# Optimization experiments

Hardware: AMD Instinct MI355X
Metric: run time of the kernel (lower is better)

## Reference

```python
import jax, jax.numpy as jnp
import numpy as np

SAMPLES = 300000
B = 256
D = 128
NEG = 1024
TEMP = 0.07
MOMENTUM = 0.5
EPS = 1e-12


def _l2n(x):
    # torch F.normalize(p=2, dim=1) semantics
    n = jnp.sqrt(jnp.sum(x * x, axis=-1, keepdims=True))
    return x / jnp.maximum(n, EPS)


def setup_inputs() -> dict:
    key = jax.random.key(0)
    k1, k2, k3, k4, k5, k6 = jax.random.split(key, 6)
    return {
        "audio_emb": jax.random.normal(k1, (B, D), dtype=jnp.float32),
        "video_emb": jax.random.normal(k2, (B, D), dtype=jnp.float32),
        "audio_memory": _l2n(jax.random.normal(k3, (SAMPLES, D), dtype=jnp.float32)),
        "video_memory": _l2n(jax.random.normal(k4, (SAMPLES, D), dtype=jnp.float32)),
        "indices": jax.random.randint(k5, (B,), 0, SAMPLES, dtype=jnp.int64),
        "neg_samples": jax.random.randint(k6, (B, NEG), 0, SAMPLES - 1, dtype=jnp.int64),
    }


def _scores(ctx, pos, neg):
    # ctx [B,D], pos [B,D], neg [B,NEG,D] -> [B, 1+NEG]
    s_pos = jnp.sum(pos * ctx, axis=-1, keepdims=True) / TEMP           # [B,1]
    s_neg = jnp.einsum("bnd,bd->bn", neg, ctx) / TEMP                   # [B,NEG]
    return jnp.concatenate([s_pos, s_neg], axis=1)


def reference(audio_emb, video_emb, audio_memory, video_memory, indices, neg_samples):
    na = _l2n(audio_emb)  # [B,D]
    nv = _l2n(video_emb)

    # alias sampling over uniform probs == uniform randint; shift to skip positive
    neg_idx = neg_samples + (neg_samples >= indices[:, None]).astype(neg_samples.dtype)

    pos_a = audio_memory[indices]      # [B,D]
    pos_v = video_memory[indices]
    neg_a = audio_memory[neg_idx]      # [B,NEG,D]
    neg_v = video_memory[neg_idx]

    # score order: (inter)audio_video, (inter)video_audio, (intra)audio, (intra)video
    scores = jnp.stack([
        _scores(na, pos_v, neg_v),
        _scores(nv, pos_a, neg_a),
        _scores(na, pos_a, neg_a),
        _scores(nv, pos_v, neg_v),
    ], axis=0)  # [4, B, 1+NEG]

    # momentum memory update (no-grad in original): gather -> mix -> normalize -> scatter
    new_a = _l2n(pos_a * MOMENTUM + na * (1.0 - MOMENTUM))
    new_v = _l2n(pos_v * MOMENTUM + nv * (1.0 - MOMENTUM))
    audio_memory_new = audio_memory.at[indices].set(new_a)
    video_memory_new = video_memory.at[indices].set(new_v)

    return scores, audio_memory_new, video_memory_new
```

## Files before the change

kernel.cpp:

```cpp
#include <hip/hip_runtime.h>

#define B 256
#define D 128
#define NEG 1024
#define SAMPLES 300000
#define TEMP 0.07f
#define EPS 1e-12f

constexpr int SCORES_ELEMS = 4 * B * (NEG + 1);
constexpr int MEM_ELEMS    = SAMPLES * D;

__device__ inline float wave_reduce_sum(float x) {
    #pragma unroll
    for (int off = 32; off > 0; off >>= 1) x += __shfl_xor(x, off, 64);
    return x;
}

__global__ __launch_bounds__(64) void prep_kernel(
    const float* __restrict__ audio_emb, const float* __restrict__ video_emb,
    const float* __restrict__ a_mem, const float* __restrict__ v_mem,
    const int* __restrict__ indices,
    float* __restrict__ na, float* __restrict__ nv,
    float* __restrict__ new_a, float* __restrict__ new_v,
    float* __restrict__ scores)
{
    const int b = blockIdx.x;
    const int l = threadIdx.x;

    float2 a = ((const float2*)(audio_emb + b * D))[l];
    float2 v = ((const float2*)(video_emb + b * D))[l];

    float sa = wave_reduce_sum(a.x * a.x + a.y * a.y);
    float sv = wave_reduce_sum(v.x * v.x + v.y * v.y);
    float ira = 1.0f / fmaxf(sqrtf(sa), EPS);
    float irv = 1.0f / fmaxf(sqrtf(sv), EPS);
    float2 naf = {a.x * ira, a.y * ira};
    float2 nvf = {v.x * irv, v.y * irv};
    ((float2*)(na + b * D))[l] = naf;
    ((float2*)(nv + b * D))[l] = nvf;

    const long long idx = (long long)indices[b];
    float2 pa = ((const float2*)(a_mem + idx * D))[l];
    float2 pv = ((const float2*)(v_mem + idx * D))[l];

    float d0 = wave_reduce_sum(pv.x * naf.x + pv.y * naf.y);
    float d1 = wave_reduce_sum(pa.x * nvf.x + pa.y * nvf.y);
    float d2 = wave_reduce_sum(pa.x * naf.x + pa.y * naf.y);
    float d3 = wave_reduce_sum(pv.x * nvf.x + pv.y * nvf.y);
    if (l == 0) {
        scores[(0 * B + b) * (NEG + 1)] = d0 / TEMP;
        scores[(1 * B + b) * (NEG + 1)] = d1 / TEMP;
        scores[(2 * B + b) * (NEG + 1)] = d2 / TEMP;
        scores[(3 * B + b) * (NEG + 1)] = d3 / TEMP;
    }

    float2 ta = {0.5f * (pa.x + naf.x), 0.5f * (pa.y + naf.y)};
    float2 tv = {0.5f * (pv.x + nvf.x), 0.5f * (pv.y + nvf.y)};
    float sta = wave_reduce_sum(ta.x * ta.x + ta.y * ta.y);
    float stv = wave_reduce_sum(tv.x * tv.x + tv.y * tv.y);
    float irta = 1.0f / fmaxf(sqrtf(sta), EPS);
    float irtv = 1.0f / fmaxf(sqrtf(stv), EPS);
    ta.x *= irta; ta.y *= irta;
    tv.x *= irtv; tv.y *= irtv;
    ((float2*)(new_a + b * D))[l] = ta;
    ((float2*)(new_v + b * D))[l] = tv;
}

__global__ __launch_bounds__(256) void neg_scores_kernel(
    const float* __restrict__ a_mem, const float* __restrict__ v_mem,
    const int* __restrict__ indices, const int* __restrict__ neg_samples,
    const float* __restrict__ na, const float* __restrict__ nv,
    float* __restrict__ scores)
{
    const int b    = blockIdx.y;
    const int hw   = threadIdx.x >> 5;
    const int lane = threadIdx.x & 31;
    const int n    = blockIdx.x * 8 + hw;

    const int pos = indices[b];
    const int ns  = neg_samples[b * NEG + n];
    const long long ni = (long long)ns + (ns >= pos ? 1 : 0);

    float4 A  = ((const float4*)(a_mem + ni * D))[lane];
    float4 V  = ((const float4*)(v_mem + ni * D))[lane];
    float4 NA = ((const float4*)(na + (long long)b * D))[lane];
    float4 NV = ((const float4*)(nv + (long long)b * D))[lane];

    float s0 = V.x * NA.x + V.y * NA.y + V.z * NA.z + V.w * NA.w;
    float s1 = A.x * NV.x + A.y * NV.y + A.z * NV.z + A.w * NV.w;
    float s2 = A.x * NA.x + A.y * NA.y + A.z * NA.z + A.w * NA.w;
    float s3 = V.x * NV.x + V.y * NV.y + V.z * NV.z + V.w * NV.w;

    #pragma unroll
    for (int off = 16; off > 0; off >>= 1) {
        s0 += __shfl_xor(s0, off, 64);
        s1 += __shfl_xor(s1, off, 64);
        s2 += __shfl_xor(s2, off, 64);
        s3 += __shfl_xor(s3, off, 64);
    }
    if (lane == 0) {
        scores[(0 * B + b) * (NEG + 1) + 1 + n] = s0 / TEMP;
        scores[(1 * B + b) * (NEG + 1) + 1 + n] = s1 / TEMP;
        scores[(2 * B + b) * (NEG + 1) + 1 + n] = s2 / TEMP;
        scores[(3 * B + b) * (NEG + 1) + 1 + n] = s3 / TEMP;
    }
}

__global__ __launch_bounds__(256) void copy_kernel(
    const float4* __restrict__ a_mem, const float4* __restrict__ v_mem,
    float4* __restrict__ out_a, float4* __restrict__ out_v, int n4)
{
    int i = blockIdx.x * blockDim.x + threadIdx.x;
    if (i < n4) {
        out_a[i] = a_mem[i];
    } else {
        i -= n4;
        if (i < n4) out_v[i] = v_mem[i];
    }
}

__global__ __launch_bounds__(128) void scatter_kernel(
    const int* __restrict__ indices,
    const float* __restrict__ new_a, const float* __restrict__ new_v,
    float* __restrict__ out_a, float* __restrict__ out_v)
{
    const int b = blockIdx.x;
    const int t = threadIdx.x;
    const int myidx = indices[b];

    __shared__ int skip;
    if (t == 0) skip = 0;
    __syncthreads();
    for (int b2 = b + 1 + t; b2 < B; b2 += blockDim.x)
        if (indices[b2] == myidx) skip = 1;
    __syncthreads();
    if (skip) return;

    out_a[(long long)myidx * D + t] = new_a[b * D + t];
    out_v[(long long)myidx * D + t] = new_v[b * D + t];
}

extern "C" void kernel_launch(void* const* d_in, const int* in_sizes, int n_in,
                              void* d_out, int out_size, void* d_ws, size_t ws_size,
                              hipStream_t stream) {
    const float* audio_emb   = (const float*)d_in[0];
    const float* video_emb   = (const float*)d_in[1];
    const float* a_mem       = (const float*)d_in[2];
    const float* v_mem       = (const float*)d_in[3];
    const int*   indices     = (const int*)d_in[4];
    const int*   neg_samples = (const int*)d_in[5];

    float* out    = (float*)d_out;
    float* scores = out;
    float* out_a  = out + SCORES_ELEMS;
    float* out_v  = out_a + MEM_ELEMS;

    float* ws    = (float*)d_ws;
    float* na    = ws;
    float* nv    = na + B * D;
    float* new_a = nv + B * D;
    float* new_v = new_a + B * D;

    prep_kernel<<<B, 64, 0, stream>>>(audio_emb, video_emb, a_mem, v_mem, indices,
                                      na, nv, new_a, new_v, scores);

    dim3 g2(NEG / 8, B);
    neg_scores_kernel<<<g2, 256, 0, stream>>>(a_mem, v_mem, indices, neg_samples,
                                              na, nv, scores);

    const int n4 = MEM_ELEMS / 4;
    copy_kernel<<<(2 * n4) / 256, 256, 0, stream>>>((const float4*)a_mem, (const float4*)v_mem,
                                                    (float4*)out_a, (float4*)out_v, n4);

    scatter_kernel<<<B, D, 0, stream>>>(indices, new_a, new_v, out_a, out_v);
}
```

Baseline: 542.8 us.

## Bucket negative indices by row block and fuse memory copy with negative scoring

Adds a counting pass that uses atomics to sort every (batch, negative) pair into buckets of 32 memory rows, each capped at 96 entries. A fused kernel then streams each row block once: it copies the block to the output memories, stages it in LDS, and computes the four negative scores for every entry in that bucket from LDS. This removes the separate random gather of memory rows for negative scoring and reuses the bandwidth already spent on the mandatory copy. In exchange it adds two small kernels, atomics and workspace, and any bucket holding more than 96 entries would silently drop scores. The old path is kept as a fallback when the workspace is too small.

```diff
diff --git a/kernel.cpp b/kernel.cpp
--- a/kernel.cpp
+++ b/kernel.cpp
@@ -6,6 +6,10 @@
 #define SAMPLES 300000
 #define TEMP 0.07f
 #define EPS 1e-12f
+
+#define ROWS_PER_BLK 32
+#define NBUCKETS (SAMPLES / ROWS_PER_BLK)
+#define CAP 96
 
 constexpr int SCORES_ELEMS = 4 * B * (NEG + 1);
 constexpr int MEM_ELEMS    = SAMPLES * D;
@@ -66,6 +70,95 @@
     ((float2*)(new_v + b * D))[l] = tv;
 }
 
+
+__global__ __launch_bounds__(256) void zero_cnt_kernel(int* __restrict__ cnt) {
+    int i = blockIdx.x * blockDim.x + threadIdx.x;
+    if (i < NBUCKETS) cnt[i] = 0;
+}
+
+__global__ __launch_bounds__(256) void fill_entries_kernel(
+    const int* __restrict__ indices, const int* __restrict__ neg_samples,
+    int* __restrict__ cnt, unsigned int* __restrict__ entries)
+{
+    int i = blockIdx.x * blockDim.x + threadIdx.x;
+    if (i >= B * NEG) return;
+    const int b = i >> 10;
+    const int n = i & (NEG - 1);
+    const int pos = indices[b];
+    const int ns  = neg_samples[i];
+    const int ni  = ns + (ns >= pos ? 1 : 0);
+    const int bucket = ni >> 5;
+    const int r      = ni & 31;
+    const int slot = atomicAdd(&cnt[bucket], 1);
+    if (slot < CAP)
+        entries[bucket * CAP + slot] =
+            (unsigned)b | ((unsigned)n << 8) | ((unsigned)r << 18);
+}
+
+__global__ __launch_bounds__(256) void fused_copy_score_kernel(
+    const float* __restrict__ a_mem, const float* __restrict__ v_mem,
+    const float* __restrict__ na, const float* __restrict__ nv,
+    const int* __restrict__ cnt, const unsigned int* __restrict__ entries,
+    float* __restrict__ out_a, float* __restrict__ out_v,
+    float* __restrict__ scores)
+{
+    __shared__ float lds_a[ROWS_PER_BLK][D];
+    __shared__ float lds_v[ROWS_PER_BLK][D];
+
+    const int k = blockIdx.x;
+    const int t = threadIdx.x;
+    const long long base = (long long)k * ROWS_PER_BLK * D;
+
+    const float4* ga = (const float4*)(a_mem + base);
+    const float4* gv = (const float4*)(v_mem + base);
+    float4* oa = (float4*)(out_a + base);
+    float4* ov = (float4*)(out_v + base);
+    float4* la = (float4*)&lds_a[0][0];
+    float4* lv = (float4*)&lds_v[0][0];
+
+    #pragma unroll
+    for (int j = 0; j < 4; ++j) {
+        const int i = j * 256 + t;
+        float4 x = ga[i]; oa[i] = x; la[i] = x;
+        float4 y = gv[i]; ov[i] = y; lv[i] = y;
+    }
+    __syncthreads();
+
+    const int ne = min(cnt[k], CAP);
+    const int w = t >> 6, lane = t & 63;
+    for (int e = w; e < ne; e += 4) {
+        const unsigned int ent = entries[k * CAP + e];
+        const int b = ent & 255;
+        const int n = (ent >> 8) & (NEG - 1);
+        const int r = ent >> 18;
+
+        float2 A  = ((const float2*)&lds_a[r][0])[lane];
+        float2 V  = ((const float2*)&lds_v[r][0])[lane];
+        float2 NA = ((const float2*)(na + b * D))[lane];
+        float2 NV = ((const float2*)(nv + b * D))[lane];
+
+        float s0 = V.x * NA.x + V.y * NA.y;
+        float s1 = A.x * NV.x + A.y * NV.y;
+        float s2 = A.x * NA.x + A.y * NA.y;
+        float s3 = V.x * NV.x + V.y * NV.y;
+
+        #pragma unroll
+        for (int off = 32; off > 0; off >>= 1) {
+            s0 += __shfl_xor(s0, off, 64);
+            s1 += __shfl_xor(s1, off, 64);
+            s2 += __shfl_xor(s2, off, 64);
+            s3 += __shfl_xor(s3, off, 64);
+        }
+        if (lane == 0) {
+            scores[(0 * B + b) * (NEG + 1) + 1 + n] = s0 / TEMP;
+            scores[(1 * B + b) * (NEG + 1) + 1 + n] = s1 / TEMP;
+            scores[(2 * B + b) * (NEG + 1) + 1 + n] = s2 / TEMP;
+            scores[(3 * B + b) * (NEG + 1) + 1 + n] = s3 / TEMP;
+        }
+    }
+}
+
+
 __global__ __launch_bounds__(256) void neg_scores_kernel(
     const float* __restrict__ a_mem, const float* __restrict__ v_mem,
     const int* __restrict__ indices, const int* __restrict__ neg_samples,
@@ -160,17 +253,32 @@
     float* nv    = na + B * D;
     float* new_a = nv + B * D;
     float* new_v = new_a + B * D;
+    int*          cnt     = (int*)(new_v + B * D);
+    unsigned int* entries = (unsigned int*)(cnt + NBUCKETS);
+
+    const size_t ws_needed = (size_t)(4 * B * D) * sizeof(float)
+                           + (size_t)NBUCKETS * sizeof(int)
+                           + (size_t)NBUCKETS * CAP * sizeof(unsigned int);
 
     prep_kernel<<<B, 64, 0, stream>>>(audio_emb, video_emb, a_mem, v_mem, indices,
                                       na, nv, new_a, new_v, scores);
 
-    dim3 g2(NEG / 8, B);
-    neg_scores_kernel<<<g2, 256, 0, stream>>>(a_mem, v_mem, indices, neg_samples,
-                                              na, nv, scores);
-
-    const int n4 = MEM_ELEMS / 4;
-    copy_kernel<<<(2 * n4) / 256, 256, 0, stream>>>((const float4*)a_mem, (const float4*)v_mem,
-                                                    (float4*)out_a, (float4*)out_v, n4);
+    if (ws_size >= ws_needed) {
+        zero_cnt_kernel<<<(NBUCKETS + 255) / 256, 256, 0, stream>>>(cnt);
+        fill_entries_kernel<<<(B * NEG) / 256, 256, 0, stream>>>(indices, neg_samples,
+                                                                 cnt, entries);
+        fused_copy_score_kernel<<<NBUCKETS, 256, 0, stream>>>(a_mem, v_mem, na, nv,
+                                                              cnt, entries,
+                                                              out_a, out_v, scores);
+    } else {
+        dim3 g2(NEG / 8, B);
+        neg_scores_kernel<<<g2, 256, 0, stream>>>(a_mem, v_mem, indices, neg_samples,
+                                                  na, nv, scores);
+        const int n4 = MEM_ELEMS / 4;
+        copy_kernel<<<(2 * n4) / 256, 256, 0, stream>>>((const float4*)a_mem,
+                                                        (const float4*)v_mem,
+                                                        (float4*)out_a, (float4*)out_v, n4);
+    }
 
     scatter_kernel<<<B, D, 0, stream>>>(indices, new_a, new_v, out_a, out_v);
 }
```

After: 556.6 us. 1.03x slower.
